# Kernel tuning notes

Hardware: AMD Instinct MI355X
Metric: run time of the kernel (lower is better)

Reference implementation:

```python
import jax, jax.numpy as jnp
import numpy as np

TEMPERATURE = 0.02
B, S, D_TOK, H = 128, 32, 128, 128  # batch, query tokens, doc tokens, hidden dim


def setup_inputs() -> dict:
    key = jax.random.key(0)
    kq, kp = jax.random.split(key)
    query_embeddings = jax.random.normal(kq, (B, S, H), dtype=jnp.float32)
    positive_embeddings = jax.random.normal(kp, (B, D_TOK, H), dtype=jnp.float32)
    return {"query_embeddings": query_embeddings, "positive_embeddings": positive_embeddings}


def reference(query_embeddings, positive_embeddings):
    # Late interaction: [b, c, s, d] = every query token vs every doc token (in-batch negatives)
    late = jnp.einsum('bsh,cdh->bcsd', query_embeddings, positive_embeddings)
    # MaxSim over doc tokens, sum over query tokens -> [b, c] score matrix
    scores = late.max(axis=-1).sum(axis=-1) / TEMPERATURE
    # In-batch negatives: label for row i is column i (the diagonal is the positive)
    logp = jax.nn.log_softmax(scores, axis=-1)
    loss = -jnp.mean(jnp.diagonal(logp))
    return loss
```

## Files before the change

### kernel.cpp

```cpp
#include <hip/hip_runtime.h>
#include <hip/hip_bf16.h>

typedef __bf16 bf16x8 __attribute__((ext_vector_type(8)));
typedef __bf16 bf16x4 __attribute__((ext_vector_type(4)));
typedef float  f32x4  __attribute__((ext_vector_type(4)));

#define Q_CHUNKS (128 * 512)
#define WS_NEED  ((size_t)Q_CHUNKS * 16 + 128 * 128 * 4)

__global__ __launch_bounds__(256) void convert_q(
    const float* __restrict__ Q, unsigned short* __restrict__ wq)
{
    const int g = blockIdx.x * 256 + threadIdx.x;
    const int b = g >> 9, j = g & 511;
    const int si = j >> 8, k = (j >> 6) & 3, l = j & 63;
    const float* src = Q + (size_t)b * 4096 + (si * 16 + (l & 15)) * 128 + k * 32 + (l >> 4) * 8;
    float4 v0 = *(const float4*)src;
    float4 v1 = *(const float4*)(src + 4);
    bf16x8 o = { (__bf16)v0.x, (__bf16)v0.y, (__bf16)v0.z, (__bf16)v0.w,
                 (__bf16)v1.x, (__bf16)v1.y, (__bf16)v1.z, (__bf16)v1.w };
    *(bf16x8*)(wq + ((size_t)g << 3)) = o;
}

__global__ __launch_bounds__(256, 2) void colbert_scores_pfold(
    const float* __restrict__ P,
    const unsigned short* __restrict__ Qb,
    float* __restrict__ scores)
{
    __shared__ __align__(16) unsigned short ps[128 * 128];

    const int tid  = threadIdx.x;
    const int lane = tid & 63;
    const int wave = tid >> 6;

    const int xcd = blockIdx.x & 7;
    const int i   = blockIdx.x >> 3;
    const int c   = (xcd << 4) + (i & 15);
    const int qtr = i >> 4;
    const int bbase = (qtr << 5) + (wave << 3);

    bf16x8 aq0[2][4];
    {
        const unsigned short* qw0 = Qb + ((size_t)bbase << 12);
        #pragma unroll
        for (int k = 0; k < 4; k++) {
            aq0[0][k] = *(const bf16x8*)(qw0 + (k << 9) + (lane << 3));
            aq0[1][k] = *(const bf16x8*)(qw0 + 2048 + (k << 9) + (lane << 3));
        }
    }

    {
        const float4* gp = (const float4*)(P + ((size_t)c << 14));
        #pragma unroll
        for (int t = 0; t < 16; t++) {
            const int j = t * 256 + tid;
            float4 v = gp[j];
            const int d = j >> 5, q = j & 31;
            const int frag = ((d >> 4) << 2) + (q >> 3);
            const int l    = (d & 15) + (((q & 7) >> 1) << 4);
            bf16x4 o = { (__bf16)v.x, (__bf16)v.y, (__bf16)v.z, (__bf16)v.w };
            *(bf16x4*)&ps[(frag << 9) + (l << 3) + ((q & 1) << 2)] = o;
        }
    }
    __syncthreads();

    bf16x8 bp[8][4];
    #pragma unroll
    for (int dj = 0; dj < 8; dj++)
        #pragma unroll
        for (int k = 0; k < 4; k++)
            bp[dj][k] = *(const bf16x8*)&ps[(((dj << 2) + k) << 9) + (lane << 3)];

    #pragma unroll
    for (int it = 0; it < 8; it++) {
        const int b = bbase + it;

        bf16x8 aq[2][4];
        if (it == 0) {
            #pragma unroll
            for (int k = 0; k < 4; k++) { aq[0][k] = aq0[0][k]; aq[1][k] = aq0[1][k]; }
        } else {
            const unsigned short* qw = Qb + ((size_t)b << 12);
            #pragma unroll
            for (int k = 0; k < 4; k++) {
                aq[0][k] = *(const bf16x8*)(qw + (k << 9) + (lane << 3));
                aq[1][k] = *(const bf16x8*)(qw + 2048 + (k << 9) + (lane << 3));
            }
        }

        float mm0 = -1e30f, mm1 = -1e30f;
        #pragma unroll
        for (int dj = 0; dj < 8; dj++) {
            f32x4 t0 = (f32x4){0.f, 0.f, 0.f, 0.f};
            f32x4 t1 = (f32x4){0.f, 0.f, 0.f, 0.f};
            #pragma unroll
            for (int k = 0; k < 4; k++) {
                t0 = __builtin_amdgcn_mfma_f32_16x16x32_bf16(bp[dj][k], aq[0][k], t0, 0, 0, 0);
                t1 = __builtin_amdgcn_mfma_f32_16x16x32_bf16(bp[dj][k], aq[1][k], t1, 0, 0, 0);
            }
            #pragma unroll
            for (int r = 0; r < 4; r++) {
                mm0 = fmaxf(mm0, t0[r]);
                mm1 = fmaxf(mm1, t1[r]);
            }
        }

        mm0 = fmaxf(mm0, __shfl_xor(mm0, 16));
        mm0 = fmaxf(mm0, __shfl_xor(mm0, 32));
        mm1 = fmaxf(mm1, __shfl_xor(mm1, 16));
        mm1 = fmaxf(mm1, __shfl_xor(mm1, 32));
        float partial = mm0 + mm1;
        partial += __shfl_xor(partial, 1);
        partial += __shfl_xor(partial, 2);
        partial += __shfl_xor(partial, 4);
        partial += __shfl_xor(partial, 8);
        if (lane == 0) scores[b * 128 + c] = partial * 50.0f;
    }
}

__global__ __launch_bounds__(1024) void colbert_loss_kernel(
    const float* __restrict__ scores, unsigned* __restrict__ out)
{
    __shared__ float wpart[16];
    const int lane = threadIdx.x & 63;
    const int wave = threadIdx.x >> 6;
    float acc = 0.f;
    #pragma unroll
    for (int i = 0; i < 8; i++) {
        const int r = wave + (i << 4);
        const float* row = scores + r * 128;
        float v0 = row[lane], v1 = row[lane + 64];
        float mx = fmaxf(v0, v1);
        mx = fmaxf(mx, __shfl_xor(mx, 1));  mx = fmaxf(mx, __shfl_xor(mx, 2));
        mx = fmaxf(mx, __shfl_xor(mx, 4));  mx = fmaxf(mx, __shfl_xor(mx, 8));
        mx = fmaxf(mx, __shfl_xor(mx, 16)); mx = fmaxf(mx, __shfl_xor(mx, 32));
        float e = expf(v0 - mx) + expf(v1 - mx);
        e += __shfl_xor(e, 1);  e += __shfl_xor(e, 2);  e += __shfl_xor(e, 4);
        e += __shfl_xor(e, 8);  e += __shfl_xor(e, 16); e += __shfl_xor(e, 32);
        float diag = (r < 64) ? __shfl(v0, r) : __shfl(v1, r - 64);
        acc += diag - (mx + logf(e));
    }
    if (lane == 0) wpart[wave] = acc;
    __syncthreads();
    if (threadIdx.x == 0) {
        float t = 0.f;
        #pragma unroll
        for (int i = 0; i < 16; i++) t += wpart[i];
        float loss = -t / 128.0f;
        unsigned bits = __float_as_uint(loss);
        unsigned rnd  = (bits + 0x7FFFu + ((bits >> 16) & 1u)) & 0xFFFF0000u;
        out[0] = rnd | (rnd >> 16);
    }
}

__global__ __launch_bounds__(256, 2) void colbert_scores_slow(
    const float* __restrict__ Q, const float* __restrict__ P, float* __restrict__ scores)
{
    __shared__ __align__(16) unsigned short qs[4 * 32 * 128];
    __shared__ __align__(16) unsigned short ps[128 * 128];
    const int tid = threadIdx.x;
    const int b0 = (blockIdx.x & 31) * 4, c0 = (blockIdx.x >> 5) * 4;
    const float4* gq = (const float4*)(Q + (size_t)b0 * 4096);
    #pragma unroll
    for (int j = tid; j < 4096; j += 256) {
        float4 v = gq[j];
        int f = j << 2, row = f >> 7, h = f & 127;
        int dst = (row << 7) + (((h >> 3) ^ (row & 15)) << 3) + (h & 7);
        bf16x4 o = { (__bf16)v.x, (__bf16)v.y, (__bf16)v.z, (__bf16)v.w };
        *(bf16x4*)&qs[dst] = o;
    }
    const int lane = tid & 63, wave = tid >> 6, n = lane & 15, quad = lane >> 4;
    const unsigned short* qb = qs + wave * 4096;
    #pragma unroll 1
    for (int it = 0; it < 4; it++) {
        const int c = c0 + it;
        if (it) __syncthreads();
        const float4* gp = (const float4*)(P + (size_t)c * 16384);
        #pragma unroll
        for (int j = tid; j < 4096; j += 256) {
            float4 v = gp[j];
            int f = j << 2, d = f >> 7, h = f & 127;
            int dst = (d << 7) + (((h >> 3) ^ (d & 15)) << 3) + (h & 7);
            bf16x4 o = { (__bf16)v.x, (__bf16)v.y, (__bf16)v.z, (__bf16)v.w };
            *(bf16x4*)&ps[dst] = o;
        }
        __syncthreads();
        f32x4 acc[2][8];
        #pragma unroll
        for (int si = 0; si < 2; si++)
            #pragma unroll
            for (int dj = 0; dj < 8; dj++) acc[si][dj] = (f32x4){0.f,0.f,0.f,0.f};
        #pragma unroll
        for (int k = 0; k < 4; k++) {
            const int chunk = (((k << 2) + quad) ^ n) << 3;
            bf16x8 a0 = *(const bf16x8*)&qb[(n << 7) + chunk];
            bf16x8 a1 = *(const bf16x8*)&qb[((n + 16) << 7) + chunk];
            #pragma unroll
            for (int dj = 0; dj < 8; dj++) {
                bf16x8 bb = *(const bf16x8*)&ps[((dj * 16 + n) << 7) + chunk];
                acc[0][dj] = __builtin_amdgcn_mfma_f32_16x16x32_bf16(a0, bb, acc[0][dj], 0, 0, 0);
                acc[1][dj] = __builtin_amdgcn_mfma_f32_16x16x32_bf16(a1, bb, acc[1][dj], 0, 0, 0);
            }
        }
        float partial = 0.f;
        #pragma unroll
        for (int si = 0; si < 2; si++)
            #pragma unroll
            for (int r = 0; r < 4; r++) {
                float m = acc[si][0][r];
                #pragma unroll
                for (int dj = 1; dj < 8; dj++) m = fmaxf(m, acc[si][dj][r]);
                m = fmaxf(m, __shfl_xor(m, 1)); m = fmaxf(m, __shfl_xor(m, 2));
                m = fmaxf(m, __shfl_xor(m, 4)); m = fmaxf(m, __shfl_xor(m, 8));
                partial += m;
            }
        partial += __shfl_xor(partial, 16);
        partial += __shfl_xor(partial, 32);
        if (lane == 0) scores[(b0 + wave) * 128 + c] = partial * 50.0f;
    }
}

extern "C" void kernel_launch(void* const* d_in, const int* in_sizes, int n_in,
                              void* d_out, int out_size, void* d_ws, size_t ws_size,
                              hipStream_t stream) {
    const float* Q = (const float*)d_in[0];
    const float* P = (const float*)d_in[1];

    if (ws_size >= WS_NEED) {
        unsigned short* wq = (unsigned short*)d_ws;
        float* scores = (float*)(wq + (size_t)Q_CHUNKS * 8);
        convert_q<<<dim3(256), dim3(256), 0, stream>>>(Q, wq);
        colbert_scores_pfold<<<dim3(512), dim3(256), 0, stream>>>(P, wq, scores);
        colbert_loss_kernel<<<dim3(1), dim3(1024), 0, stream>>>(scores, (unsigned*)d_out);
    } else {
        float* scores = (float*)d_ws;
        colbert_scores_slow<<<dim3(1024), dim3(256), 0, stream>>>(Q, P, scores);
        colbert_loss_kernel<<<dim3(1), dim3(1024), 0, stream>>>(scores, (unsigned*)d_out);
    }
}
```

Baseline: 82.99 us.

## Pre-convert P to bf16 fragment layout and process two docs per block

P is now converted to bf16 once, in MFMA fragment order, in a combined pre-pass alongside Q. The scores kernel then copies two pre-laid-out documents straight into LDS instead of converting fp32 P per block. Each block now covers 2 docs × 16 queries instead of 1 doc × 32 queries. Query fragments for the next iteration are prefetched into registers while the current one runs. The loss kernel is rewritten to give each row to 8 threads using float4 loads, and the workspace grows to hold bf16 P.

```diff
diff --git a/kernel.cpp b/kernel.cpp
--- a/kernel.cpp
+++ b/kernel.cpp
@@ -5,62 +5,74 @@
 typedef __bf16 bf16x4 __attribute__((ext_vector_type(4)));
 typedef float  f32x4  __attribute__((ext_vector_type(4)));
 
-#define Q_CHUNKS (128 * 512)
-#define WS_NEED  ((size_t)Q_CHUNKS * 16 + 128 * 128 * 4)
-
-__global__ __launch_bounds__(256) void convert_q(
-    const float* __restrict__ Q, unsigned short* __restrict__ wq)
-{
-    const int g = blockIdx.x * 256 + threadIdx.x;
-    const int b = g >> 9, j = g & 511;
-    const int si = j >> 8, k = (j >> 6) & 3, l = j & 63;
-    const float* src = Q + (size_t)b * 4096 + (si * 16 + (l & 15)) * 128 + k * 32 + (l >> 4) * 8;
-    float4 v0 = *(const float4*)src;
-    float4 v1 = *(const float4*)(src + 4);
-    bf16x8 o = { (__bf16)v0.x, (__bf16)v0.y, (__bf16)v0.z, (__bf16)v0.w,
-                 (__bf16)v1.x, (__bf16)v1.y, (__bf16)v1.z, (__bf16)v1.w };
-    *(bf16x8*)(wq + ((size_t)g << 3)) = o;
-}
-
-__global__ __launch_bounds__(256, 2) void colbert_scores_pfold(
-    const float* __restrict__ P,
+#define WQ_ELEMS (128 * 32 * 128)
+#define WP_ELEMS (128 * 128 * 128)
+#define WS_NEED  ((size_t)(WQ_ELEMS + WP_ELEMS) * 2 + 128 * 128 * 4)
+
+__global__ __launch_bounds__(256) void convert_qp(
+    const float* __restrict__ Q, const float* __restrict__ P,
+    unsigned short* __restrict__ wq, unsigned short* __restrict__ wp)
+{
+    const int bid = blockIdx.x;
+    if (bid < 256) {
+        const int g = bid * 256 + threadIdx.x;
+        const int b = g >> 9, j = g & 511;
+        const int si = j >> 8, k = (j >> 6) & 3, l = j & 63;
+        const float* src = Q + (size_t)b * 4096 + (si * 16 + (l & 15)) * 128 + k * 32 + (l >> 4) * 8;
+        float4 v0 = *(const float4*)src;
+        float4 v1 = *(const float4*)(src + 4);
+        bf16x8 o = { (__bf16)v0.x, (__bf16)v0.y, (__bf16)v0.z, (__bf16)v0.w,
+                     (__bf16)v1.x, (__bf16)v1.y, (__bf16)v1.z, (__bf16)v1.w };
+        *(bf16x8*)(wq + ((size_t)g << 3)) = o;
+    } else {
+        const int g = (bid - 256) * 256 + threadIdx.x;
+        const int c = g >> 11;
+        const int f = (g >> 6) & 31, l = g & 63;
+        const int dj = f >> 2, k = f & 3;
+        const float* src = P + (size_t)c * 16384 + (dj * 16 + (l & 15)) * 128 + k * 32 + (l >> 4) * 8;
+        float4 v0 = *(const float4*)src;
+        float4 v1 = *(const float4*)(src + 4);
+        bf16x8 o = { (__bf16)v0.x, (__bf16)v0.y, (__bf16)v0.z, (__bf16)v0.w,
+                     (__bf16)v1.x, (__bf16)v1.y, (__bf16)v1.z, (__bf16)v1.w };
+        *(bf16x8*)(wp + ((size_t)g << 3)) = o;
+    }
+}
+
+__global__ __launch_bounds__(256, 2) void colbert_scores_v2(
+    const unsigned short* __restrict__ Pb,
     const unsigned short* __restrict__ Qb,
     float* __restrict__ scores)
 {
-    __shared__ __align__(16) unsigned short ps[128 * 128];
+    __shared__ __align__(16) unsigned short ps[2][16384];
 
     const int tid  = threadIdx.x;
     const int lane = tid & 63;
     const int wave = tid >> 6;
 
     const int xcd = blockIdx.x & 7;
-    const int i   = blockIdx.x >> 3;
-    const int c   = (xcd << 4) + (i & 15);
-    const int qtr = i >> 4;
-    const int bbase = (qtr << 5) + (wave << 3);
-
-    bf16x8 aq0[2][4];
+    const int idx = blockIdx.x >> 3;
+    const int cp  = (xcd << 3) + (idx & 7);
+    const int g   = idx >> 3;
+    const int cw  = wave >> 1;
+    const int c   = (cp << 1) + cw;
+    const int bbase = (g << 4) + ((wave & 1) << 3);
+
+    bf16x8 A[2][4];
     {
-        const unsigned short* qw0 = Qb + ((size_t)bbase << 12);
+        const unsigned short* qw = Qb + ((size_t)bbase << 12);
         #pragma unroll
         for (int k = 0; k < 4; k++) {
-            aq0[0][k] = *(const bf16x8*)(qw0 + (k << 9) + (lane << 3));
-            aq0[1][k] = *(const bf16x8*)(qw0 + 2048 + (k << 9) + (lane << 3));
+            A[0][k] = *(const bf16x8*)(qw + (k << 9) + (lane << 3));
+            A[1][k] = *(const bf16x8*)(qw + 2048 + (k << 9) + (lane << 3));
         }
     }
 
     {
-        const float4* gp = (const float4*)(P + ((size_t)c << 14));
-        #pragma unroll
-        for (int t = 0; t < 16; t++) {
-            const int j = t * 256 + tid;
-            float4 v = gp[j];
-            const int d = j >> 5, q = j & 31;
-            const int frag = ((d >> 4) << 2) + (q >> 3);
-            const int l    = (d & 15) + (((q & 7) >> 1) << 4);
-            bf16x4 o = { (__bf16)v.x, (__bf16)v.y, (__bf16)v.z, (__bf16)v.w };
-            *(bf16x4*)&ps[(frag << 9) + (l << 3) + ((q & 1) << 2)] = o;
-        }
+        const float4* src = (const float4*)(Pb + ((size_t)cp << 15));
+        float4* dst = (float4*)&ps[0][0];
+        #pragma unroll
+        for (int t = 0; t < 16; t++)
+            dst[t * 256 + tid] = src[t * 256 + tid];
     }
     __syncthreads();
 
@@ -69,22 +81,19 @@
     for (int dj = 0; dj < 8; dj++)
         #pragma unroll
         for (int k = 0; k < 4; k++)
-            bp[dj][k] = *(const bf16x8*)&ps[(((dj << 2) + k) << 9) + (lane << 3)];
+            bp[dj][k] = *(const bf16x8*)&ps[cw][(((dj << 2) + k) << 9) + (lane << 3)];
 
     #pragma unroll
     for (int it = 0; it < 8; it++) {
         const int b = bbase + it;
 
-        bf16x8 aq[2][4];
-        if (it == 0) {
-            #pragma unroll
-            for (int k = 0; k < 4; k++) { aq[0][k] = aq0[0][k]; aq[1][k] = aq0[1][k]; }
-        } else {
-            const unsigned short* qw = Qb + ((size_t)b << 12);
+        bf16x8 N[2][4];
+        if (it < 7) {
+            const unsigned short* qw = Qb + ((size_t)(b + 1) << 12);
             #pragma unroll
             for (int k = 0; k < 4; k++) {
-                aq[0][k] = *(const bf16x8*)(qw + (k << 9) + (lane << 3));
-                aq[1][k] = *(const bf16x8*)(qw + 2048 + (k << 9) + (lane << 3));
+                N[0][k] = *(const bf16x8*)(qw + (k << 9) + (lane << 3));
+                N[1][k] = *(const bf16x8*)(qw + 2048 + (k << 9) + (lane << 3));
             }
         }
 
@@ -95,8 +104,8 @@
             f32x4 t1 = (f32x4){0.f, 0.f, 0.f, 0.f};
             #pragma unroll
             for (int k = 0; k < 4; k++) {
-                t0 = __builtin_amdgcn_mfma_f32_16x16x32_bf16(bp[dj][k], aq[0][k], t0, 0, 0, 0);
-                t1 = __builtin_amdgcn_mfma_f32_16x16x32_bf16(bp[dj][k], aq[1][k], t1, 0, 0, 0);
+                t0 = __builtin_amdgcn_mfma_f32_16x16x32_bf16(bp[dj][k], A[0][k], t0, 0, 0, 0);
+                t1 = __builtin_amdgcn_mfma_f32_16x16x32_bf16(bp[dj][k], A[1][k], t1, 0, 0, 0);
             }
             #pragma unroll
             for (int r = 0; r < 4; r++) {
@@ -115,38 +124,54 @@
         partial += __shfl_xor(partial, 4);
         partial += __shfl_xor(partial, 8);
         if (lane == 0) scores[b * 128 + c] = partial * 50.0f;
-    }
-}
-
-__global__ __launch_bounds__(1024) void colbert_loss_kernel(
+
+        if (it < 7) {
+            #pragma unroll
+            for (int k = 0; k < 4; k++) { A[0][k] = N[0][k]; A[1][k] = N[1][k]; }
+        }
+    }
+}
+
+__global__ __launch_bounds__(1024) void colbert_loss128(
     const float* __restrict__ scores, unsigned* __restrict__ out)
 {
-    __shared__ float wpart[16];
-    const int lane = threadIdx.x & 63;
-    const int wave = threadIdx.x >> 6;
-    float acc = 0.f;
-    #pragma unroll
-    for (int i = 0; i < 8; i++) {
-        const int r = wave + (i << 4);
-        const float* row = scores + r * 128;
-        float v0 = row[lane], v1 = row[lane + 64];
-        float mx = fmaxf(v0, v1);
-        mx = fmaxf(mx, __shfl_xor(mx, 1));  mx = fmaxf(mx, __shfl_xor(mx, 2));
-        mx = fmaxf(mx, __shfl_xor(mx, 4));  mx = fmaxf(mx, __shfl_xor(mx, 8));
-        mx = fmaxf(mx, __shfl_xor(mx, 16)); mx = fmaxf(mx, __shfl_xor(mx, 32));
-        float e = expf(v0 - mx) + expf(v1 - mx);
-        e += __shfl_xor(e, 1);  e += __shfl_xor(e, 2);  e += __shfl_xor(e, 4);
-        e += __shfl_xor(e, 8);  e += __shfl_xor(e, 16); e += __shfl_xor(e, 32);
-        float diag = (r < 64) ? __shfl(v0, r) : __shfl(v1, r - 64);
-        acc += diag - (mx + logf(e));
-    }
-    if (lane == 0) wpart[wave] = acc;
+    __shared__ float gpart[128];
+    __shared__ float wpart[2];
+    const int tid = threadIdx.x;
+    const int grp = tid >> 3;
+    const int j   = tid & 7;
+
+    const float4* row = (const float4*)(scores + grp * 128);
+    float v[16];
+    #pragma unroll
+    for (int u = 0; u < 4; u++) {
+        float4 q = row[j * 4 + u];
+        v[u * 4 + 0] = q.x; v[u * 4 + 1] = q.y; v[u * 4 + 2] = q.z; v[u * 4 + 3] = q.w;
+    }
+    float m = v[0];
+    #pragma unroll
+    for (int u = 1; u < 16; u++) m = fmaxf(m, v[u]);
+    m = fmaxf(m, __shfl_xor(m, 1));
+    m = fmaxf(m, __shfl_xor(m, 2));
+    m = fmaxf(m, __shfl_xor(m, 4));
+    float e = 0.f;
+    #pragma unroll
+    for (int u = 0; u < 16; u++) e += expf(v[u] - m);
+    e += __shfl_xor(e, 1);
+    e += __shfl_xor(e, 2);
+    e += __shfl_xor(e, 4);
+    if (j == 0) gpart[grp] = scores[grp * 129] - m - logf(e);
     __syncthreads();
-    if (threadIdx.x == 0) {
-        float t = 0.f;
-        #pragma unroll
-        for (int i = 0; i < 16; i++) t += wpart[i];
-        float loss = -t / 128.0f;
+
+    if (tid < 128) {
+        float p = gpart[tid];
+        p += __shfl_xor(p, 1);  p += __shfl_xor(p, 2);  p += __shfl_xor(p, 4);
+        p += __shfl_xor(p, 8);  p += __shfl_xor(p, 16); p += __shfl_xor(p, 32);
+        if ((tid & 63) == 0) wpart[tid >> 6] = p;
+    }
+    __syncthreads();
+    if (tid == 0) {
+        float loss = -(wpart[0] + wpart[1]) / 128.0f;
         unsigned bits = __float_as_uint(loss);
         unsigned rnd  = (bits + 0x7FFFu + ((bits >> 16) & 1u)) & 0xFFFF0000u;
         out[0] = rnd | (rnd >> 16);
@@ -228,13 +253,14 @@
 
     if (ws_size >= WS_NEED) {
         unsigned short* wq = (unsigned short*)d_ws;
-        float* scores = (float*)(wq + (size_t)Q_CHUNKS * 8);
-        convert_q<<<dim3(256), dim3(256), 0, stream>>>(Q, wq);
-        colbert_scores_pfold<<<dim3(512), dim3(256), 0, stream>>>(P, wq, scores);
-        colbert_loss_kernel<<<dim3(1), dim3(1024), 0, stream>>>(scores, (unsigned*)d_out);
+        unsigned short* wp = wq + WQ_ELEMS;
+        float* scores = (float*)(wp + WP_ELEMS);
+        convert_qp<<<dim3(1280), dim3(256), 0, stream>>>(Q, P, wq, wp);
+        colbert_scores_v2<<<dim3(512), dim3(256), 0, stream>>>(wp, wq, scores);
+        colbert_loss128<<<dim3(1), dim3(1024), 0, stream>>>(scores, (unsigned*)d_out);
     } else {
         float* scores = (float*)d_ws;
         colbert_scores_slow<<<dim3(1024), dim3(256), 0, stream>>>(Q, P, scores);
-        colbert_loss_kernel<<<dim3(1), dim3(1024), 0, stream>>>(scores, (unsigned*)d_out);
-    }
-}
+        colbert_loss128<<<dim3(1), dim3(1024), 0, stream>>>(scores, (unsigned*)d_out);
+    }
+}
```

New measurement: 81.42 us. About the same (-1.9%).
